# Kernel tuning notes

Hardware: AMD Instinct MI355X
Metric: run time of the kernel (lower is better)

The kernel has to match this reference:

```python
import jax, jax.numpy as jnp
import numpy as np

N_NODES = 50000

def _graph_conv(x, src, dst, W, b, n):
    # DGL GraphConv, norm='both': D_dst^{-1/2} * sum_edges(D_src^{-1/2} * (x W)) + b
    xw = x @ W  # [N, out]
    ones = jnp.ones(src.shape, jnp.float32)
    deg_out = jnp.maximum(jax.ops.segment_sum(ones, src, num_segments=n), 1.0)
    deg_in = jnp.maximum(jax.ops.segment_sum(ones, dst, num_segments=n), 1.0)
    norm_src = deg_out ** -0.5
    norm_dst = deg_in ** -0.5
    msg = xw[src] * norm_src[src][:, None]          # [E, out] gather
    agg = jax.ops.segment_sum(msg, dst, num_segments=n)  # [N, out] scatter-add
    return agg * norm_dst[:, None] + b


def _rgcn_layer(x, src, dst, W, b, n):
    # HeteroGraphConv with aggregate='sum' over relations
    out = _graph_conv(x, src[0], dst[0], W[0], b[0], n)
    for r in range(1, src.shape[0]):
        out = out + _graph_conv(x, src[r], dst[r], W[r], b[r], n)
    return out


def setup_inputs() -> dict:
    key = jax.random.key(0)
    ks = jax.random.split(key, 9)
    R, E = 3, 200000
    din, dhid, dout = 128, 128, 64
    x = jax.random.normal(ks[0], (N_NODES, din), jnp.float32)
    src = jax.random.randint(ks[1], (R, E), 0, N_NODES, jnp.int32)
    dst = jax.random.randint(ks[2], (R, E), 0, N_NODES, jnp.int32)
    neg_src = jax.random.randint(ks[3], (E,), 0, N_NODES, jnp.int32)
    neg_dst = jax.random.randint(ks[4], (E,), 0, N_NODES, jnp.int32)
    W1 = jax.random.normal(ks[5], (R, din, dhid), jnp.float32) / np.sqrt(din)
    b1 = jnp.zeros((R, dhid), jnp.float32)
    W2 = jax.random.normal(ks[6], (R, dhid, dout), jnp.float32) / np.sqrt(dhid)
    b2 = jnp.zeros((R, dout), jnp.float32)
    return {"x": x, "src": src, "dst": dst, "neg_src": neg_src,
            "neg_dst": neg_dst, "W1": W1, "b1": b1, "W2": W2, "b2": b2}


def reference(x, src, dst, neg_src, neg_dst, W1, b1, W2, b2):
    n = x.shape[0]
    h = jax.nn.relu(_rgcn_layer(x, src, dst, W1, b1, n))
    h = _rgcn_layer(h, src, dst, W2, b2, n)  # [N, out]
    # HeteroDotProductPredictor on etype = relation 0 (u_dot_v -> [E, 1])
    pos = jnp.sum(h[src[0]] * h[dst[0]], axis=-1, keepdims=True)
    neg = jnp.sum(h[neg_src] * h[neg_dst], axis=-1, keepdims=True)
    return pos, neg
```

## Files before the change

### kernel.cpp

```cpp
#include <hip/hip_runtime.h>

#define N_NODES 50000
#define E_EDGES 200000
#define R_REL 3
#define D_IN 128
#define D_HID 128
#define D_OUT 64
#define N_SCAN (R_REL * N_NODES)
#define BCAP 16
#define OVCAP 4096
#define NBE 2344
#define NBP 1563

typedef __attribute__((ext_vector_type(8))) short bf16x8;
typedef __attribute__((ext_vector_type(4))) float f32x4;

__device__ inline unsigned short f2bf(float v) {
    union { float f; unsigned int u; } x; x.f = v;
    unsigned int r = x.u + 0x7fffu + ((x.u >> 16) & 1u);
    return (unsigned short)(r >> 16);
}
__device__ inline float bf2f(unsigned short h) {
    union { unsigned int u; float f; } x; x.u = ((unsigned int)h) << 16; return x.f;
}
__device__ inline float bf_lo(unsigned int p) {
    union { unsigned int u; float f; } x; x.u = p << 16; return x.f;
}
__device__ inline float bf_hi(unsigned int p) {
    union { unsigned int u; float f; } x; x.u = p & 0xffff0000u; return x.f;
}

__global__ __launch_bounds__(256) void k_zero_i32(int* __restrict__ p, int n) {
    int i = blockIdx.x * 256 + threadIdx.x;
    if (i < n) p[i] = 0;
}

__global__ __launch_bounds__(256) void k_count_prep(const int* __restrict__ src,
                                                    const int* __restrict__ dst,
                                                    const float* __restrict__ x,
                                                    const float* __restrict__ W1,
                                                    const float* __restrict__ W2,
                                                    const float* __restrict__ b1,
                                                    int* __restrict__ deg_out,
                                                    int* __restrict__ cnt_in,
                                                    int* __restrict__ ov_cnt,
                                                    uint2* __restrict__ ovlist,
                                                    int* __restrict__ bucket,
                                                    unsigned int* __restrict__ xb,
                                                    unsigned short* __restrict__ w1t_h,
                                                    unsigned short* __restrict__ w1t_l,
                                                    unsigned short* __restrict__ w2t_h,
                                                    unsigned short* __restrict__ w2t_l,
                                                    float* __restrict__ bsum) {
    int g = blockIdx.x / 5;
    int m = blockIdx.x % 5;
    int t = threadIdx.x;
    if (m < 3) {
        int eb = g * 3 + m;
        int i = eb * 256 + t;
        if (i >= R_REL * E_EDGES) return;
        int r = i / E_EDGES;
        int s = src[i];
        int d = dst[i];
        atomicAdd(&deg_out[r * N_NODES + s], 1);
        int bin = r * N_NODES + d;
        int pos = atomicAdd(&cnt_in[bin], 1);
        if (pos < BCAP) {
            bucket[bin * BCAP + pos] = s;
        } else {
            int oi = atomicAdd(ov_cnt, 1);
            if (oi < OVCAP) {
                uint2 e;
                e.x = (unsigned int)bin;
                e.y = (unsigned int)s;
                ovlist[oi] = e;
            }
        }
    } else {
        int pb = g * 2 + (m - 3);
        int i = pb * 256 + t;
        if (i < 400000) {
#pragma unroll
            for (int k = 0; k < 4; k++) {
                int q = i * 4 + k;
                float4 v = ((const float4*)x)[q];
                uint2 u;
                u.x = ((unsigned int)f2bf(v.y) << 16) | f2bf(v.x);
                u.y = ((unsigned int)f2bf(v.w) << 16) | f2bf(v.z);
                ((uint2*)xb)[q] = u;
            }
        }
        if (i < R_REL * D_IN * D_HID) {
            int r = i >> 14;
            int kk = (i >> 7) & 127;
            int c = i & 127;
            float v = W1[i];
            unsigned short h = f2bf(v);
            unsigned short l = f2bf(v - bf2f(h));
            int o = r * 16384 + c * 128 + kk;
            w1t_h[o] = h;
            w1t_l[o] = l;
        }
        if (i < R_REL * D_HID * D_OUT) {
            int r = i >> 13;
            int kk = (i >> 6) & 127;
            int cl = i & 63;
            float v = W2[i];
            unsigned short h = f2bf(v);
            unsigned short l = f2bf(v - bf2f(h));
            int o = (r * 64 + cl) * 128 + kk;
            w2t_h[o] = h;
            w2t_l[o] = l;
        }
        if (i < 128) bsum[i] = b1[i] + b1[128 + i] + b1[256 + i];
    }
}

__global__ __launch_bounds__(256) void k_rednorm(const int* __restrict__ deg_out,
                                                 const int* __restrict__ cnt_in,
                                                 float* __restrict__ norm_out,
                                                 float* __restrict__ norm_in) {
    int b = blockIdx.x * 256 + threadIdx.x;
    if (b >= N_SCAN) return;
    int o = deg_out[b];
    int d = cnt_in[b];
    norm_out[b] = rsqrtf((float)(o > 1 ? o : 1));
    norm_in[b] = rsqrtf((float)(d > 1 ? d : 1));
}

__global__ __launch_bounds__(256) void k_aggall(const int* __restrict__ cnt_in,
                                                const int* __restrict__ bucket,
                                                const float* __restrict__ norm_out,
                                                const float* __restrict__ norm_in,
                                                const int* __restrict__ ov_cnt,
                                                const uint2* __restrict__ ovlist,
                                                const unsigned int* __restrict__ xb,
                                                unsigned int* __restrict__ aggh) {
    int w = (blockIdx.x * 256 + threadIdx.x) >> 6;
    if (w >= N_NODES) return;
    int r = blockIdx.y;
    int lane = threadIdx.x & 63;
    const unsigned int* tab = xb + lane;
    const float* nout = norm_out + r * N_NODES;
    int bin = r * N_NODES + w;
    int n = cnt_in[bin];
    const uint4* bp = (const uint4*)(bucket + bin * BCAP);
    uint4 q0 = bp[0], q1 = bp[1], q2 = bp[2], q3 = bp[3];
    unsigned int sl[16] = {q0.x, q0.y, q0.z, q0.w, q1.x, q1.y, q1.z, q1.w,
                           q2.x, q2.y, q2.z, q2.w, q3.x, q3.y, q3.z, q3.w};
    int nn = n < BCAP ? n : BCAP;
    float ax = 0.f, ay = 0.f;
#pragma unroll
    for (int j = 0; j < BCAP; j++) {
        if (j < nn) {
            unsigned int s = sl[j];
            float c = nout[s];
            unsigned int p = tab[s * 64];
            ax += c * bf_lo(p);
            ay += c * bf_hi(p);
        }
    }
    int oc = *ov_cnt;
    if (oc > 0) {
        if (oc > OVCAP) oc = OVCAP;
        for (int k = 0; k < oc; k++) {
            uint2 e = ovlist[k];
            if ((int)e.x == bin) {
                float c = nout[e.y];
                unsigned int p = tab[e.y * 64];
                ax += c * bf_lo(p);
                ay += c * bf_hi(p);
            }
        }
    }
    float ni = norm_in[bin];
    unsigned int o = ((unsigned int)f2bf(ay * ni) << 16) | f2bf(ax * ni);
    aggh[bin * 64 + lane] = o;
}

__global__ __launch_bounds__(256) void k_mm1f(const unsigned short* __restrict__ aggh,
                                              const unsigned short* __restrict__ wt_h,
                                              const unsigned short* __restrict__ wt_l,
                                              const float* __restrict__ bsum,
                                              unsigned short* __restrict__ h1h,
                                              unsigned short* __restrict__ h1l,
                                              int M) {
    __shared__ short sA[2048];
    __shared__ short sWh[4096], sWl[4096];
    int t = threadIdx.x;
    int row0 = blockIdx.x * 64;
    int wid = t >> 6;
    int lane = t & 63;
    int lr = lane & 15;
    int lkg = lane >> 4;
    int wr = (wid & 1) * 32;
    int wc = (wid >> 1) * 64;

    f32x4 acc[2][4];
#pragma unroll
    for (int i = 0; i < 2; i++)
#pragma unroll
        for (int j = 0; j < 4; j++) acc[i][j] = (f32x4)(0.f);

    int arow = t >> 2;
    int akg = t & 3;

    for (int k0 = 0; k0 < 384; k0 += 32) {
        int rr = k0 >> 7;
        int kk = k0 & 127;
        {
            int gr = row0 + arow;
            int cidx = akg * 64 + arow;
            if (gr < M)
                *(bf16x8*)&sA[cidx * 8] =
                    *(const bf16x8*)&aggh[(rr * N_NODES + gr) * 128 + kk + akg * 8];
            else
                *(bf16x8*)&sA[cidx * 8] = (bf16x8)(short)0;
        }
#pragma unroll
        for (int itr = 0; itr < 2; itr++) {
            int cc = t + itr * 256;
            int col = cc >> 2;
            int kg = cc & 3;
            int go = rr * 16384 + col * 128 + kk + kg * 8;
            int cidx = kg * 128 + col;
            *(bf16x8*)&sWh[cidx * 8] = *(const bf16x8*)&wt_h[go];
            *(bf16x8*)&sWl[cidx * 8] = *(const bf16x8*)&wt_l[go];
        }
        __syncthreads();
        bf16x8 a[2], bh[4], bl[4];
#pragma unroll
        for (int i = 0; i < 2; i++) {
            int cidx = lkg * 64 + wr + i * 16 + lr;
            a[i] = *(const bf16x8*)&sA[cidx * 8];
        }
#pragma unroll
        for (int j = 0; j < 4; j++) {
            int cidx = lkg * 128 + wc + j * 16 + lr;
            bh[j] = *(const bf16x8*)&sWh[cidx * 8];
            bl[j] = *(const bf16x8*)&sWl[cidx * 8];
        }
#pragma unroll
        for (int i = 0; i < 2; i++)
#pragma unroll
            for (int j = 0; j < 4; j++) {
                acc[i][j] = __builtin_amdgcn_mfma_f32_16x16x32_bf16(a[i], bh[j], acc[i][j], 0, 0, 0);
                acc[i][j] = __builtin_amdgcn_mfma_f32_16x16x32_bf16(a[i], bl[j], acc[i][j], 0, 0, 0);
            }
        __syncthreads();
    }
#pragma unroll
    for (int i = 0; i < 2; i++)
#pragma unroll
        for (int q = 0; q < 4; q++) {
            int gr = row0 + wr + i * 16 + lkg * 4 + q;
            if (gr >= M) continue;
#pragma unroll
            for (int j = 0; j < 4; j++) {
                int gc = wc + j * 16 + lr;
                float u = fmaxf(acc[i][j][q] + bsum[gc], 0.f);
                unsigned short h = f2bf(u);
                h1h[gr * 128 + gc] = h;
                h1l[gr * 128 + gc] = f2bf(u - bf2f(h));
            }
        }
}

__global__ __launch_bounds__(256) void k_mm2(const unsigned short* __restrict__ h1h,
                                             const unsigned short* __restrict__ h1l,
                                             const unsigned short* __restrict__ wt_h,
                                             const unsigned short* __restrict__ wt_l,
                                             const float* __restrict__ norm_out,
                                             unsigned short* __restrict__ xwb2, int M) {
    __shared__ short sAh[2048], sAl[2048];
    __shared__ short sWh[6144], sWl[6144];
    int t = threadIdx.x;
    int row0 = blockIdx.x * 64;
    int wid = t >> 6;
    int lane = t & 63;
    int lr = lane & 15;
    int lkg = lane >> 4;
    int wr = (wid & 1) * 32;
    int wc = (wid >> 1) * 96;

    f32x4 acc[2][6];
#pragma unroll
    for (int i = 0; i < 2; i++)
#pragma unroll
        for (int j = 0; j < 6; j++) acc[i][j] = (f32x4)(0.f);

    int arow = t >> 2;
    int akg = t & 3;

    for (int k0 = 0; k0 < 128; k0 += 32) {
        {
            int gr = row0 + arow;
            int cidx = akg * 64 + arow;
            if (gr < M) {
                int go = gr * 128 + k0 + akg * 8;
                *(bf16x8*)&sAh[cidx * 8] = *(const bf16x8*)&h1h[go];
                *(bf16x8*)&sAl[cidx * 8] = *(const bf16x8*)&h1l[go];
            } else {
                *(bf16x8*)&sAh[cidx * 8] = (bf16x8)(short)0;
                *(bf16x8*)&sAl[cidx * 8] = (bf16x8)(short)0;
            }
        }
#pragma unroll
        for (int itr = 0; itr < 3; itr++) {
            int cc = t + itr * 256;
            int col = cc >> 2;
            int kg = cc & 3;
            int go = col * 128 + k0 + kg * 8;
            int cidx = kg * 192 + col;
            *(bf16x8*)&sWh[cidx * 8] = *(const bf16x8*)&wt_h[go];
            *(bf16x8*)&sWl[cidx * 8] = *(const bf16x8*)&wt_l[go];
        }
        __syncthreads();
        bf16x8 ah[2], al[2];
#pragma unroll
        for (int i = 0; i < 2; i++) {
            int cidx = lkg * 64 + wr + i * 16 + lr;
            ah[i] = *(const bf16x8*)&sAh[cidx * 8];
            al[i] = *(const bf16x8*)&sAl[cidx * 8];
        }
#pragma unroll
        for (int j = 0; j < 6; j++) {
            int cidx = lkg * 192 + wc + j * 16 + lr;
            bf16x8 bh = *(const bf16x8*)&sWh[cidx * 8];
            bf16x8 bl = *(const bf16x8*)&sWl[cidx * 8];
#pragma unroll
            for (int i = 0; i < 2; i++) {
                acc[i][j] = __builtin_amdgcn_mfma_f32_16x16x32_bf16(ah[i], bh, acc[i][j], 0, 0, 0);
                acc[i][j] = __builtin_amdgcn_mfma_f32_16x16x32_bf16(ah[i], bl, acc[i][j], 0, 0, 0);
                acc[i][j] = __builtin_amdgcn_mfma_f32_16x16x32_bf16(al[i], bh, acc[i][j], 0, 0, 0);
            }
        }
        __syncthreads();
    }
#pragma unroll
    for (int i = 0; i < 2; i++)
#pragma unroll
        for (int q = 0; q < 4; q++) {
            int gr = row0 + wr + i * 16 + lkg * 4 + q;
            if (gr >= M) continue;
#pragma unroll
            for (int j = 0; j < 6; j++) {
                int gc = wc + j * 16 + lr;
                float sc = norm_out[(gc >> 6) * N_NODES + gr];
                xwb2[gr * 192 + gc] = f2bf(acc[i][j][q] * sc);
            }
        }
}

__global__ __launch_bounds__(256) void k_agg64f(const int* __restrict__ cnt_in,
                                                const int* __restrict__ bucket,
                                                const float* __restrict__ norm_in,
                                                const int* __restrict__ ov_cnt,
                                                const uint2* __restrict__ ovlist,
                                                const unsigned short* __restrict__ xwb,
                                                const float* __restrict__ b2,
                                                unsigned short* __restrict__ h2b) {
    int w = (blockIdx.x * 256 + threadIdx.x) >> 6;
    if (w >= N_NODES) return;
    int lane = threadIdx.x & 63;
    float acc = b2[lane] + b2[64 + lane] + b2[128 + lane];
    int oc = *ov_cnt;
    if (oc > OVCAP) oc = OVCAP;
#pragma unroll
    for (int r = 0; r < R_REL; r++) {
        const unsigned short* tab = xwb + r * 64 + lane;
        int bin = r * N_NODES + w;
        int n = cnt_in[bin];
        const uint4* bp = (const uint4*)(bucket + bin * BCAP);
        uint4 q0 = bp[0], q1 = bp[1], q2 = bp[2], q3 = bp[3];
        unsigned int sl[16] = {q0.x, q0.y, q0.z, q0.w, q1.x, q1.y, q1.z, q1.w,
                               q2.x, q2.y, q2.z, q2.w, q3.x, q3.y, q3.z, q3.w};
        int nn = n < BCAP ? n : BCAP;
        float a = 0.f;
#pragma unroll
        for (int j = 0; j < BCAP; j++) {
            if (j < nn) a += bf2f(tab[sl[j] * 192]);
        }
        if (oc > 0) {
            for (int k = 0; k < oc; k++) {
                uint2 e = ovlist[k];
                if ((int)e.x == bin) a += bf2f(tab[e.y * 192]);
            }
        }
        acc += norm_in[bin] * a;
    }
    h2b[w * 64 + lane] = f2bf(acc);
}

__global__ __launch_bounds__(256) void k_predict(const int* __restrict__ sa,
                                                 const int* __restrict__ sb,
                                                 const int* __restrict__ na,
                                                 const int* __restrict__ nb,
                                                 const unsigned short* __restrict__ h2b,
                                                 float* __restrict__ out) {
    int tid = blockIdx.x * 256 + threadIdx.x;
    int p = tid >> 4;
    if (p >= 2 * E_EDGES) return;
    int lane = tid & 15;
    int ia, ib;
    if (p < E_EDGES) { ia = sa[p]; ib = sb[p]; }
    else             { ia = na[p - E_EDGES]; ib = nb[p - E_EDGES]; }
    uint2 ua = *(const uint2*)&h2b[ia * 64 + lane * 4];
    uint2 ub = *(const uint2*)&h2b[ib * 64 + lane * 4];
    float d = bf_lo(ua.x) * bf_lo(ub.x) + bf_hi(ua.x) * bf_hi(ub.x)
            + bf_lo(ua.y) * bf_lo(ub.y) + bf_hi(ua.y) * bf_hi(ub.y);
    d += __shfl_xor(d, 1);
    d += __shfl_xor(d, 2);
    d += __shfl_xor(d, 4);
    d += __shfl_xor(d, 8);
    if (lane == 0) out[p] = d;
}


extern "C" void kernel_launch(void* const* d_in, const int* in_sizes, int n_in,
                              void* d_out, int out_size, void* d_ws, size_t ws_size,
                              hipStream_t stream) {
    (void)in_sizes; (void)n_in; (void)out_size; (void)ws_size;
    const float* x       = (const float*)d_in[0];
    const int*   src     = (const int*)d_in[1];
    const int*   dst     = (const int*)d_in[2];
    const int*   neg_src = (const int*)d_in[3];
    const int*   neg_dst = (const int*)d_in[4];
    const float* W1      = (const float*)d_in[5];
    const float* b1      = (const float*)d_in[6];
    const float* W2      = (const float*)d_in[7];
    const float* b2      = (const float*)d_in[8];
    float* out = (float*)d_out;
    float* ws  = (float*)d_ws;

    float* norm_out = ws;
    float* norm_in  = ws + N_SCAN;
    int*   deg_out  = (int*)(ws + 300000);
    int*   cnt_in   = (int*)(ws + 450000);
    int*   ov_cnt   = (int*)(ws + 600000);
    uint2* ovlist   = (uint2*)(ws + 600016);
    int*   bucket   = (int*)(ws + 608208);
    unsigned short* w1t_h = (unsigned short*)(ws + 3008208);
    unsigned short* w1t_l = (unsigned short*)(ws + 3032784);
    unsigned short* w2t_h = (unsigned short*)(ws + 3057360);
    unsigned short* w2t_l = (unsigned short*)(ws + 3069648);
    float* bsum     = ws + 3081936;
    unsigned int*   aggh = (unsigned int*)(ws + 3082064);
    unsigned short* xwb2 = (unsigned short*)(ws + 3082064);
    unsigned short* h1h  = (unsigned short*)(ws + 12682064);
    unsigned short* h2b  = (unsigned short*)(ws + 12682064);
    unsigned short* h1l  = (unsigned short*)(ws + 15882064);
    unsigned int*   xb   = (unsigned int*)(ws + 15882064);

    const int NB_WAVE = (N_NODES * 64 + 255) / 256;
    const int NB_MM   = (N_NODES + 63) / 64;

    k_zero_i32<<<(300016 + 255) / 256, 256, 0, stream>>>(deg_out, 300016);
    k_count_prep<<<782 * 5, 256, 0, stream>>>(src, dst, x, W1, W2, b1,
                                              deg_out, cnt_in, ov_cnt, ovlist, bucket,
                                              xb, w1t_h, w1t_l, w2t_h, w2t_l, bsum);
    k_rednorm<<<(N_SCAN + 255) / 256, 256, 0, stream>>>(deg_out, cnt_in, norm_out, norm_in);

    dim3 gagg(NB_WAVE, R_REL);
    k_aggall<<<gagg, 256, 0, stream>>>(cnt_in, bucket, norm_out, norm_in,
                                       ov_cnt, ovlist, xb, aggh);
    k_mm1f<<<NB_MM, 256, 0, stream>>>((const unsigned short*)aggh, w1t_h, w1t_l, bsum,
                                      h1h, h1l, N_NODES);

    k_mm2<<<NB_MM, 256, 0, stream>>>(h1h, h1l, w2t_h, w2t_l, norm_out, xwb2, N_NODES);
    k_agg64f<<<NB_WAVE, 256, 0, stream>>>(cnt_in, bucket, norm_in, ov_cnt, ovlist,
                                          xwb2, b2, h2b);

    k_predict<<<(2 * E_EDGES * 16 + 255) / 256, 256, 0, stream>>>(
        src, dst, neg_src, neg_dst, h2b, out);
}
```

Measured before the change: 259.5 us.

## Split layer-1 gather by feature half and store layer-2 messages relation-major

The layer-1 aggregation kernel now launches twice as many waves: each wave handles one 64-column half of the bf16 feature row and gathers 16-bit values instead of packed pairs. All neighbor loads are issued before the accumulation loop to raise memory-level parallelism. The layer-2 message buffer is switched from interleaved [N,192] to relation-major [3][N,64], so each relation's gather reads a compact table. The x-to-bf16 conversion loop is reindexed for coalesced access. The changes trade doubled index, count and norm loads in layer 1 for smaller per-lane gathers and better locality.

```diff
diff --git a/kernel.cpp b/kernel.cpp
--- a/kernel.cpp
+++ b/kernel.cpp
@@ -9,8 +9,6 @@
 #define N_SCAN (R_REL * N_NODES)
 #define BCAP 16
 #define OVCAP 4096
-#define NBE 2344
-#define NBP 1563
 
 typedef __attribute__((ext_vector_type(8))) short bf16x8;
 typedef __attribute__((ext_vector_type(4))) float f32x4;
@@ -78,11 +76,11 @@
         }
     } else {
         int pb = g * 2 + (m - 3);
-        int i = pb * 256 + t;
-        if (i < 400000) {
-#pragma unroll
-            for (int k = 0; k < 4; k++) {
-                int q = i * 4 + k;
+        int qbase = pb * 1024;
+#pragma unroll
+        for (int k = 0; k < 4; k++) {
+            int q = qbase + k * 256 + t;
+            if (q < N_NODES * 32) {
                 float4 v = ((const float4*)x)[q];
                 uint2 u;
                 u.x = ((unsigned int)f2bf(v.y) << 16) | f2bf(v.x);
@@ -90,6 +88,7 @@
                 ((uint2*)xb)[q] = u;
             }
         }
+        int i = pb * 256 + t;
         if (i < R_REL * D_IN * D_HID) {
             int r = i >> 14;
             int kk = (i >> 7) & 127;
@@ -134,48 +133,45 @@
                                                 const float* __restrict__ norm_in,
                                                 const int* __restrict__ ov_cnt,
                                                 const uint2* __restrict__ ovlist,
-                                                const unsigned int* __restrict__ xb,
-                                                unsigned int* __restrict__ aggh) {
+                                                const unsigned short* __restrict__ xb,
+                                                unsigned short* __restrict__ aggh) {
     int w = (blockIdx.x * 256 + threadIdx.x) >> 6;
     if (w >= N_NODES) return;
     int r = blockIdx.y;
+    int h = blockIdx.z;
     int lane = threadIdx.x & 63;
-    const unsigned int* tab = xb + lane;
+    const unsigned short* tab = xb + h * 64 + lane;
     const float* nout = norm_out + r * N_NODES;
     int bin = r * N_NODES + w;
     int n = cnt_in[bin];
+    int nn = n < BCAP ? n : BCAP;
     const uint4* bp = (const uint4*)(bucket + bin * BCAP);
     uint4 q0 = bp[0], q1 = bp[1], q2 = bp[2], q3 = bp[3];
-    unsigned int sl[16] = {q0.x, q0.y, q0.z, q0.w, q1.x, q1.y, q1.z, q1.w,
-                           q2.x, q2.y, q2.z, q2.w, q3.x, q3.y, q3.z, q3.w};
-    int nn = n < BCAP ? n : BCAP;
-    float ax = 0.f, ay = 0.f;
+    unsigned int sl[BCAP] = {q0.x, q0.y, q0.z, q0.w, q1.x, q1.y, q1.z, q1.w,
+                             q2.x, q2.y, q2.z, q2.w, q3.x, q3.y, q3.z, q3.w};
+    float c[BCAP];
+    unsigned short pv[BCAP];
 #pragma unroll
     for (int j = 0; j < BCAP; j++) {
         if (j < nn) {
-            unsigned int s = sl[j];
-            float c = nout[s];
-            unsigned int p = tab[s * 64];
-            ax += c * bf_lo(p);
-            ay += c * bf_hi(p);
-        }
+            c[j] = nout[sl[j]];
+            pv[j] = tab[sl[j] * 128];
+        }
+    }
+    float a = 0.f;
+#pragma unroll
+    for (int j = 0; j < BCAP; j++) {
+        if (j < nn) a += c[j] * bf2f(pv[j]);
     }
     int oc = *ov_cnt;
     if (oc > 0) {
         if (oc > OVCAP) oc = OVCAP;
         for (int k = 0; k < oc; k++) {
             uint2 e = ovlist[k];
-            if ((int)e.x == bin) {
-                float c = nout[e.y];
-                unsigned int p = tab[e.y * 64];
-                ax += c * bf_lo(p);
-                ay += c * bf_hi(p);
-            }
-        }
-    }
-    float ni = norm_in[bin];
-    unsigned int o = ((unsigned int)f2bf(ay * ni) << 16) | f2bf(ax * ni);
-    aggh[bin * 64 + lane] = o;
+            if ((int)e.x == bin) a += nout[e.y] * bf2f(tab[e.y * 128]);
+        }
+    }
+    aggh[bin * 128 + h * 64 + lane] = f2bf(a * norm_in[bin]);
 }
 
 __global__ __launch_bounds__(256) void k_mm1f(const unsigned short* __restrict__ aggh,
@@ -346,8 +342,10 @@
 #pragma unroll
             for (int j = 0; j < 6; j++) {
                 int gc = wc + j * 16 + lr;
-                float sc = norm_out[(gc >> 6) * N_NODES + gr];
-                xwb2[gr * 192 + gc] = f2bf(acc[i][j][q] * sc);
+                int rr = gc >> 6;
+                int cl = gc & 63;
+                float sc = norm_out[rr * N_NODES + gr];
+                xwb2[rr * (N_NODES * 64) + gr * 64 + cl] = f2bf(acc[i][j][q] * sc);
             }
         }
 }
@@ -368,23 +366,28 @@
     if (oc > OVCAP) oc = OVCAP;
 #pragma unroll
     for (int r = 0; r < R_REL; r++) {
-        const unsigned short* tab = xwb + r * 64 + lane;
+        const unsigned short* tab = xwb + r * (N_NODES * 64) + lane;
         int bin = r * N_NODES + w;
         int n = cnt_in[bin];
         const uint4* bp = (const uint4*)(bucket + bin * BCAP);
         uint4 q0 = bp[0], q1 = bp[1], q2 = bp[2], q3 = bp[3];
-        unsigned int sl[16] = {q0.x, q0.y, q0.z, q0.w, q1.x, q1.y, q1.z, q1.w,
-                               q2.x, q2.y, q2.z, q2.w, q3.x, q3.y, q3.z, q3.w};
+        unsigned int sl[BCAP] = {q0.x, q0.y, q0.z, q0.w, q1.x, q1.y, q1.z, q1.w,
+                                 q2.x, q2.y, q2.z, q2.w, q3.x, q3.y, q3.z, q3.w};
         int nn = n < BCAP ? n : BCAP;
+        unsigned short pv[BCAP];
+#pragma unroll
+        for (int j = 0; j < BCAP; j++) {
+            if (j < nn) pv[j] = tab[sl[j] * 64];
+        }
         float a = 0.f;
 #pragma unroll
         for (int j = 0; j < BCAP; j++) {
-            if (j < nn) a += bf2f(tab[sl[j] * 192]);
+            if (j < nn) a += bf2f(pv[j]);
         }
         if (oc > 0) {
             for (int k = 0; k < oc; k++) {
                 uint2 e = ovlist[k];
-                if ((int)e.x == bin) a += bf2f(tab[e.y * 192]);
+                if ((int)e.x == bin) a += bf2f(tab[e.y * 64]);
             }
         }
         acc += norm_in[bin] * a;
@@ -445,7 +448,7 @@
     unsigned short* w2t_h = (unsigned short*)(ws + 3057360);
     unsigned short* w2t_l = (unsigned short*)(ws + 3069648);
     float* bsum     = ws + 3081936;
-    unsigned int*   aggh = (unsigned int*)(ws + 3082064);
+    unsigned short* aggh = (unsigned short*)(ws + 3082064);
     unsigned short* xwb2 = (unsigned short*)(ws + 3082064);
     unsigned short* h1h  = (unsigned short*)(ws + 12682064);
     unsigned short* h2b  = (unsigned short*)(ws + 12682064);
@@ -461,11 +464,10 @@
                                               xb, w1t_h, w1t_l, w2t_h, w2t_l, bsum);
     k_rednorm<<<(N_SCAN + 255) / 256, 256, 0, stream>>>(deg_out, cnt_in, norm_out, norm_in);
 
-    dim3 gagg(NB_WAVE, R_REL);
+    dim3 gagg(NB_WAVE, R_REL, 2);
     k_aggall<<<gagg, 256, 0, stream>>>(cnt_in, bucket, norm_out, norm_in,
-                                       ov_cnt, ovlist, xb, aggh);
-    k_mm1f<<<NB_MM, 256, 0, stream>>>((const unsigned short*)aggh, w1t_h, w1t_l, bsum,
-                                      h1h, h1l, N_NODES);
+                                       ov_cnt, ovlist, (const unsigned short*)xb, aggh);
+    k_mm1f<<<NB_MM, 256, 0, stream>>>(aggh, w1t_h, w1t_l, bsum, h1h, h1l, N_NODES);
 
     k_mm2<<<NB_MM, 256, 0, stream>>>(h1h, h1l, w2t_h, w2t_l, norm_out, xwb2, N_NODES);
     k_agg64f<<<NB_WAVE, 256, 0, stream>>>(cnt_in, bucket, norm_in, ov_cnt, ovlist,
```

After: 330.5 us. 27.4% more time.
